# Optimization experiments

Measured on AMD Instinct MI355X. Metric: run time of the kernel, lower is better.

Reference implementation:

```python
import jax, jax.numpy as jnp
import numpy as np

B, S, L, C, H, D, CP = 32, 4, 64, 32, 4, 8, 16  # batch, tracks, bins, c_msa, heads, d_head, c_pair


def _ln(x, g, b, eps=1e-5):
    m = jnp.mean(x, axis=-1, keepdims=True)
    v = jnp.mean((x - m) ** 2, axis=-1, keepdims=True)
    return (x - m) / jnp.sqrt(v + eps) * g + b


def setup_inputs() -> dict:
    key = jax.random.key(0)
    ks = jax.random.split(key, 20)
    n = lambda k, shape, s=0.1: jax.random.normal(k, shape, jnp.float32) * s
    return dict(
        chip_ctcf=n(ks[0], (B, L), 1.0),
        chip_hac=n(ks[1], (B, L), 1.0),
        chip_me1=n(ks[2], (B, L), 1.0),
        chip_me3=n(ks[3], (B, L), 1.0),
        bulk_map=n(ks[4], (B, 1, L, L), 1.0),
        we_w=n(ks[5], (C, 1)), we_b=jnp.zeros((C,), jnp.float32),
        pos=n(ks[6], (1, 1, L, C)),
        mn_g=jnp.ones((C,), jnp.float32), mn_b=jnp.zeros((C,), jnp.float32),
        wq=n(ks[7], (C, C)), bq=jnp.zeros((C,), jnp.float32),
        wk=n(ks[8], (C, C)), bk=jnp.zeros((C,), jnp.float32),
        wv=n(ks[9], (C, C)), bv=jnp.zeros((C,), jnp.float32),
        wo=n(ks[10], (C, C)), bo=jnp.zeros((C,), jnp.float32),
        an_g=jnp.ones((C,), jnp.float32), an_b=jnp.zeros((C,), jnp.float32),
        conv_w=n(ks[11], (H,)), conv_b=jnp.zeros((H,), jnp.float32),
        gate_w=n(ks[12], (H, D, D)), gate_b=jnp.zeros((H, D), jnp.float32),
        pp_w=n(ks[13], (CP, C * C), 0.03), pp_b=jnp.zeros((CP,), jnp.float32),
        ada_g=jnp.ones((CP,), jnp.float32), ada_b=jnp.zeros((CP,), jnp.float32),
        ada_alpha=jnp.ones((1,), jnp.float32),
    )


def reference(chip_ctcf, chip_hac, chip_me1, chip_me3, bulk_map,
              we_w, we_b, pos, mn_g, mn_b,
              wq, bq, wk, bk, wv, bv, wo, bo, an_g, an_b,
              conv_w, conv_b, gate_w, gate_b,
              pp_w, pp_b, ada_g, ada_b, ada_alpha):
    # 1) build MSA: (B, S=4, L, C)
    signals = jnp.stack([chip_ctcf, chip_hac, chip_me1, chip_me3], axis=1)  # (B,S,L)
    msa = signals[..., None] * we_w[:, 0] + we_b                            # Linear(1,C)
    x = _ln(msa + pos, mn_g, mn_b)                                          # (B,S,L,C)

    # 2) row self-attention with bulk-derived per-head bias
    q = (x @ wq.T + bq).reshape(B, S, L, H, D)
    k = (x @ wk.T + bk).reshape(B, S, L, H, D)
    v = (x @ wv.T + bv).reshape(B, S, L, H, D)
    scores = jnp.einsum('bslhd,bsmhd->bshlm', q, k) / jnp.sqrt(jnp.float32(D))
    bias = bulk_map * conv_w.reshape(1, H, 1, 1) + conv_b.reshape(1, H, 1, 1)  # 1x1 conv -> (B,H,L,L)
    attn = jax.nn.softmax(scores + bias[:, None], axis=-1)                     # (B,S,H,L,L)
    out = jnp.einsum('bshlm,bsmhd->bshld', attn, v)
    gate = jax.nn.sigmoid(jnp.einsum('hcd,bshld->bshlc', gate_w, out)
                          + gate_b[None, None, :, None, :])
    out = out * gate
    out = out.transpose(0, 1, 3, 2, 4).reshape(B, S, L, C)
    out = out @ wo.T + bo
    x = _ln(x + out, an_g, an_b)                                            # post-attn LayerNorm

    # 3) outer-product (of max over tracks) pair features
    m = jnp.max(x, axis=1)                                                  # (B,L,C)
    pair = jnp.einsum('bic,bjd->bijcd', m, m).reshape(B, L, L, C * C)       # (B,L,L,1024)
    nrm = jnp.sqrt(jnp.sum(pair * pair, axis=-1, keepdims=True))
    pair = pair / jnp.maximum(nrm, 1e-6)                                    # F.normalize
    feat = pair @ pp_w.T + pp_b                                             # (B,L,L,CP)
    feat = feat + ada_alpha * _ln(feat, ada_g, ada_b)                       # AdaNorm
    feat = jax.nn.silu(feat)
    return feat.transpose(0, 3, 1, 2)                                       # (B,CP,L,L)
```

## Files before the change

### kernel.cpp

```cpp
#include <hip/hip_runtime.h>
#include <hip/hip_bf16.h>

#define NB 32
#define NS 4
#define NL 64
#define NC 32
#define NH 4
#define ND 8
#define NCP 16

using fp = const float* __restrict__;

__global__ __launch_bounds__(512) void k1_attn(
    fp ctcf, fp hac, fp me1, fp me3, fp bulk,
    fp we_w, fp we_b, fp pos, fp mn_g, fp mn_b,
    fp wq, fp bq, fp wk, fp bk, fp wv, fp bv,
    fp wo, fp bo, fp an_g, fp an_b,
    fp conv_w, fp conv_b, fp gate_w, fp gate_b,
    float* __restrict__ xpostT)
{
    __shared__ __align__(16) float q2[NL*36];
    __shared__ __align__(16) float k2[NL*36];
    __shared__ __align__(16) float v2[NL*36];
    __shared__ __align__(16) float x2[NL*36];
    __shared__ __align__(16) float a2[16*36];
    __shared__ float bs[16*65];
    __shared__ __align__(16) float ws_wq[NC*NC];
    __shared__ __align__(16) float ws_wk[NC*NC];
    __shared__ __align__(16) float ws_wv[NC*NC];
    __shared__ __align__(16) float ws_wo[NC*NC];
    __shared__ __align__(16) float ws_gw[NH*ND*ND];
    __shared__ __align__(16) float ws_par[352];

    const int t    = threadIdx.x;
    const int w    = t >> 6;
    const int l    = t & 63;
    const int bx   = blockIdx.x;
    const int b    = bx >> 4;
    const int s    = (bx >> 2) & 3;
    const int qtr  = bx & 3;

    if (t < 256) ((float4*)ws_wq)[t]       = ((const float4*)wq)[t];
    else         ((float4*)ws_wk)[t - 256] = ((const float4*)wk)[t - 256];

    if (t < 256) ((float4*)ws_wv)[t] = ((const float4*)wv)[t];
    else {
        int u = t - 256;
        if (u < 64) ((float4*)ws_gw)[u] = ((const float4*)gate_w)[u];
        else if (u < 152){
            int p = u - 64;
            const float* sp = (p < 8)  ? we_w : (p < 16) ? we_b
                            : (p < 24) ? mn_g : (p < 32) ? mn_b
                            : (p < 40) ? bq   : (p < 48) ? bk
                            : (p < 56) ? bv   : (p < 64) ? bo
                            : (p < 72) ? an_g : (p < 80) ? an_b : gate_b;
            ((float4*)ws_par)[p] = ((const float4*)sp)[p & 7];
        }
    }
    if (t < 256){
        int c = t >> 3, k4 = t & 7;
        ((float4*)ws_wo)[c*8 + (k4 ^ ((c >> 1) & 7))] = ((const float4*)wo)[t];
    }
    if (t < 256){
        float4 v = ((const float4*)(bulk + b*NL*NL + qtr*16*NL))[t];
        int row = t >> 4, col = (t & 15) << 2;
        float* dst = &bs[row*65 + col];
        dst[0] = v.x; dst[1] = v.y; dst[2] = v.z; dst[3] = v.w;
    }

    fp sigp = (s == 0) ? ctcf : (s == 1) ? hac : (s == 2) ? me1 : me3;
    const float sig = sigp[b*NL + l];
    __syncthreads();

    const float4* pws = (const float4*)ws_par;

    float x[NC];
    float mean = 0.f;
#pragma unroll
    for (int k4 = 0; k4 < 8; k4++){
        float4 ww = pws[k4];
        float4 wb = pws[8 + k4];
        float4 pp = ((const float4*)pos)[l*8 + k4];
        x[4*k4+0] = sig*ww.x + wb.x + pp.x;
        x[4*k4+1] = sig*ww.y + wb.y + pp.y;
        x[4*k4+2] = sig*ww.z + wb.z + pp.z;
        x[4*k4+3] = sig*ww.w + wb.w + pp.w;
        mean += x[4*k4+0] + x[4*k4+1] + x[4*k4+2] + x[4*k4+3];
    }
    mean *= (1.f/NC);
    float var = 0.f;
#pragma unroll
    for (int c = 0; c < NC; c++){ float d = x[c] - mean; var += d*d; }
    var *= (1.f/NC);
    float inv = rsqrtf(var + 1e-5f);
#pragma unroll
    for (int k4 = 0; k4 < 8; k4++){
        float4 gg = pws[16 + k4];
        float4 bb = pws[24 + k4];
        x[4*k4+0] = (x[4*k4+0] - mean)*inv*gg.x + bb.x;
        x[4*k4+1] = (x[4*k4+1] - mean)*inv*gg.y + bb.y;
        x[4*k4+2] = (x[4*k4+2] - mean)*inv*gg.z + bb.z;
        x[4*k4+3] = (x[4*k4+3] - mean)*inv*gg.w + bb.w;
    }

    {
        float aqv[4], akv[4], avv[4];
#pragma unroll
        for (int e4 = 0; e4 < 4; e4++){
            const int e = (w << 2) + e4;
            float aq = ws_par[128 + e], ak = ws_par[160 + e], av = ws_par[192 + e];
#pragma unroll
            for (int k4 = 0; k4 < 8; k4++){
                float4 wq4 = *(const float4*)&ws_wq[e*NC + 4*k4];
                float4 wk4 = *(const float4*)&ws_wk[e*NC + 4*k4];
                float4 wv4 = *(const float4*)&ws_wv[e*NC + 4*k4];
                float x0 = x[4*k4+0], x1 = x[4*k4+1], x2v = x[4*k4+2], x3 = x[4*k4+3];
                aq += wq4.x*x0 + wq4.y*x1 + wq4.z*x2v + wq4.w*x3;
                ak += wk4.x*x0 + wk4.y*x1 + wk4.z*x2v + wk4.w*x3;
                av += wv4.x*x0 + wv4.y*x1 + wv4.z*x2v + wv4.w*x3;
            }
            aqv[e4] = aq; akv[e4] = ak; avv[e4] = av;
        }
        const int slt = ((w >> 1) ^ (l >> 4));
        const int kh  = (w & 1);
        const int off = l*36 + slt*8 + kh*4;
        *(float4*)&q2[off] = make_float4(aqv[0], aqv[1], aqv[2], aqv[3]);
        *(float4*)&k2[off] = make_float4(akv[0], akv[1], akv[2], akv[3]);
        *(float4*)&v2[off] = make_float4(avv[0], avv[1], avv[2], avv[3]);
        float xa = 0.f, xb2 = 0.f, xc = 0.f, xd = 0.f;
#pragma unroll
        for (int ww = 0; ww < 8; ww++)
            if (ww == w){ xa = x[4*ww]; xb2 = x[4*ww+1]; xc = x[4*ww+2]; xd = x[4*ww+3]; }
        *(float4*)&x2[l*36 + ((w ^ (l >> 4)) << 2)] = make_float4(xa, xb2, xc, xd);
    }
    __syncthreads();

    {
        const int h   = w >> 1;
        const int sub = ((w & 1) << 6) | l;
        const int rl  = sub >> 3;
        const int q8  = sub & 7;
        const int r   = qtr*16 + rl;
        const int m0  = q8 << 3;

        const int qoff = r*36 + ((h ^ (r >> 4)) << 3);
        float4 qa = *(const float4*)&q2[qoff];
        float4 qb = *(const float4*)&q2[qoff + 4];

        const float rs8 = 0.35355339059327373f;
        const float cw = conv_w[h], cb = conv_b[h];
        const float* bsr = &bs[rl*65];
        float srow[8];
        float mx = -1e30f;
#pragma unroll
        for (int mi = 0; mi < 8; mi++){
            int m  = m0 + mi;
            int kb = m*36 + ((h ^ (m >> 4)) << 3);
            float4 ka  = *(const float4*)&k2[kb];
            float4 kb4 = *(const float4*)&k2[kb + 4];
            float dot = qa.x*ka.x + qa.y*ka.y + qa.z*ka.z + qa.w*ka.w
                      + qb.x*kb4.x + qb.y*kb4.y + qb.z*kb4.z + qb.w*kb4.w;
            float vv = dot*rs8 + bsr[m]*cw + cb;
            srow[mi] = vv;
            mx = fmaxf(mx, vv);
        }
        mx = fmaxf(mx, __shfl_xor(mx, 1));
        mx = fmaxf(mx, __shfl_xor(mx, 2));
        mx = fmaxf(mx, __shfl_xor(mx, 4));
        float sm = 0.f;
#pragma unroll
        for (int mi = 0; mi < 8; mi++){ srow[mi] = __expf(srow[mi] - mx); sm += srow[mi]; }
        sm += __shfl_xor(sm, 1);
        sm += __shfl_xor(sm, 2);
        sm += __shfl_xor(sm, 4);
        float is = 1.f / sm;

        float4 oa = make_float4(0.f,0.f,0.f,0.f);
        float4 ob = make_float4(0.f,0.f,0.f,0.f);
#pragma unroll
        for (int mi = 0; mi < 8; mi++){
            int m  = m0 + mi;
            int vb = m*36 + ((h ^ (m >> 4)) << 3);
            float a = srow[mi] * is;
            float4 va  = *(const float4*)&v2[vb];
            float4 vb4 = *(const float4*)&v2[vb + 4];
            oa.x += a*va.x;  oa.y += a*va.y;  oa.z += a*va.z;  oa.w += a*va.w;
            ob.x += a*vb4.x; ob.y += a*vb4.y; ob.z += a*vb4.z; ob.w += a*vb4.w;
        }
#define RED3(f) f += __shfl_xor(f, 1); f += __shfl_xor(f, 2); f += __shfl_xor(f, 4);
        RED3(oa.x) RED3(oa.y) RED3(oa.z) RED3(oa.w)
        RED3(ob.x) RED3(ob.y) RED3(ob.z) RED3(ob.w)
#undef RED3

        const float* gwl = &ws_gw[(h*ND + q8)*ND];
        float4 g1 = *(const float4*)gwl;
        float4 g2 = *(const float4*)(gwl + 4);
        float g = ws_par[320 + h*ND + q8]
                + g1.x*oa.x + g1.y*oa.y + g1.z*oa.z + g1.w*oa.w
                + g2.x*ob.x + g2.y*ob.y + g2.z*ob.z + g2.w*ob.w;
        float oc = oa.x;
        if (q8 == 1) oc = oa.y;
        if (q8 == 2) oc = oa.z;
        if (q8 == 3) oc = oa.w;
        if (q8 == 4) oc = ob.x;
        if (q8 == 5) oc = ob.y;
        if (q8 == 6) oc = ob.z;
        if (q8 == 7) oc = ob.w;
        a2[rl*36 + h*8 + q8] = oc * (1.f/(1.f + __expf(-g)));
    }
    __syncthreads();

    {
        const int r3 = t >> 5;
        const int c  = t & 31;
        const int rg = qtr*16 + r3;
        float acc = ws_par[224 + c];
#pragma unroll
        for (int k4 = 0; k4 < 8; k4++){
            float4 av = *(const float4*)&a2[r3*36 + (k4 << 2)];
            float4 w1 = ((const float4*)ws_wo)[c*8 + (k4 ^ ((c >> 1) & 7))];
            acc += av.x*w1.x + av.y*w1.y + av.z*w1.z + av.w*w1.w;
        }
        float xr = x2[rg*36 + (((c >> 2) ^ (rg >> 4)) << 2) + (c & 3)];
        float val = xr + acc;
        float ps = val, pq = val*val;
        ps += __shfl_xor(ps, 1);  pq += __shfl_xor(pq, 1);
        ps += __shfl_xor(ps, 2);  pq += __shfl_xor(pq, 2);
        ps += __shfl_xor(ps, 4);  pq += __shfl_xor(pq, 4);
        ps += __shfl_xor(ps, 8);  pq += __shfl_xor(pq, 8);
        ps += __shfl_xor(ps, 16); pq += __shfl_xor(pq, 16);
        float mn = ps * (1.f/NC);
        float vr = pq * (1.f/NC) - mn*mn;
        float iv = rsqrtf(vr + 1e-5f);
        xpostT[((b*NS + s)*NL + rg)*NC + c] =
            (val - mn)*iv*ws_par[256 + c] + ws_par[288 + c];
    }
}

__global__ __launch_bounds__(256) void k23_pair(
    const float* __restrict__ xpostT, fp pp_w,
    fp pp_b, fp ada_g, fp ada_b, fp ada_alpha,
    float* __restrict__ out)
{
    __shared__ float ppws[8*NC*NC];
    __shared__ float mh[NC*66];
    __shared__ float u[NCP*4*NC];
    __shared__ float nrm_s[NL];

    const int b  = blockIdx.x >> 4;
    const int it = blockIdx.x & 15;
    const int t  = threadIdx.x;
    const int w  = t >> 6;
    const int j  = t & 63;

    float4 s1[8];
#pragma unroll
    for (int k = 0; k < 8; k++) s1[k] = ((const float4*)pp_w)[k*256 + t];

    const float4* xb4 = (const float4*)(xpostT + b*NS*NL*NC);
#pragma unroll
    for (int k = 0; k < 2; k++){
        int idx = k*256 + t;
        float4 v0 = xb4[idx];
        float4 v1 = xb4[512  + idx];
        float4 v2 = xb4[1024 + idx];
        float4 v3 = xb4[1536 + idx];
        float m0 = fmaxf(fmaxf(v0.x, v1.x), fmaxf(v2.x, v3.x));
        float m1 = fmaxf(fmaxf(v0.y, v1.y), fmaxf(v2.y, v3.y));
        float m2 = fmaxf(fmaxf(v0.z, v1.z), fmaxf(v2.z, v3.z));
        float m3 = fmaxf(fmaxf(v0.w, v1.w), fmaxf(v2.w, v3.w));
        int l = idx >> 3, c4 = idx & 7;
        mh[(4*c4+0)*66 + l] = m0;
        mh[(4*c4+1)*66 + l] = m1;
        mh[(4*c4+2)*66 + l] = m2;
        mh[(4*c4+3)*66 + l] = m3;
    }
#pragma unroll
    for (int k = 0; k < 8; k++) ((float4*)ppws)[k*256 + t] = s1[k];
    __syncthreads();

    if (t < NL){
        float sq = 0.f;
#pragma unroll
        for (int c = 0; c < NC; c++){ float v = mh[c*66 + t]; sq += v*v; }
        nrm_s[t] = sqrtf(sq);
    }

    float4 s2[8];
#pragma unroll
    for (int k = 0; k < 8; k++) s2[k] = ((const float4*)pp_w)[2048 + k*256 + t];

#pragma unroll
    for (int loop = 0; loop < 4; loop++){
        int idx = loop*256 + t;
        int d  = idx & 31;
        int ip = (idx >> 5) & 3;
        int pl = idx >> 7;
        int i  = it*4 + ip;
        float acc = 0.f;
#pragma unroll
        for (int c = 0; c < NC; c++)
            acc += mh[c*66 + i] * ppws[pl*1024 + c*32 + d];
        u[pl*128 + ip*32 + d] = acc;
    }
    __syncthreads();
#pragma unroll
    for (int k = 0; k < 8; k++) ((float4*)ppws)[k*256 + t] = s2[k];
    __syncthreads();

#pragma unroll
    for (int loop = 0; loop < 4; loop++){
        int idx = loop*256 + t;
        int d  = idx & 31;
        int ip = (idx >> 5) & 3;
        int pl = idx >> 7;
        int i  = it*4 + ip;
        float acc = 0.f;
#pragma unroll
        for (int c = 0; c < NC; c++)
            acc += mh[c*66 + i] * ppws[pl*1024 + c*32 + d];
        u[(8 + pl)*128 + ip*32 + d] = acc;
    }
    __syncthreads();

    float md[NC];
#pragma unroll
    for (int c = 0; c < NC; c++) md[c] = mh[c*66 + j];

    const int i = it*4 + w;
    float f[NCP];
#pragma unroll
    for (int p = 0; p < NCP; p++){
        float a = 0.f;
#pragma unroll
        for (int k4 = 0; k4 < 8; k4++){
            float4 uv = *(const float4*)&u[p*128 + w*32 + (k4 << 2)];
            a += uv.x*md[4*k4+0] + uv.y*md[4*k4+1] + uv.z*md[4*k4+2] + uv.w*md[4*k4+3];
        }
        f[p] = a;
    }

    const float sc = 1.f / fmaxf(nrm_s[i] * nrm_s[j], 1e-6f);
    const float alpha = ada_alpha[0];
    float fsum = 0.f, fsq = 0.f;
#pragma unroll
    for (int p = 0; p < NCP; p++){
        float v = f[p]*sc + pp_b[p];
        f[p] = v; fsum += v; fsq += v*v;
    }
    float fmean = fsum * (1.f/NCP);
    float fvar  = fsq * (1.f/NCP) - fmean*fmean;
    float finv  = rsqrtf(fvar + 1e-5f);
#pragma unroll
    for (int p = 0; p < NCP; p++){
        float v = f[p] + alpha * ((f[p] - fmean)*finv*ada_g[p] + ada_b[p]);
        out[((b*NCP + p)*NL + i)*NL + j] = v / (1.f + __expf(-v));
    }
}

extern "C" void kernel_launch(void* const* d_in, const int* in_sizes, int n_in,
                              void* d_out, int out_size, void* d_ws, size_t ws_size,
                              hipStream_t stream)
{
    float* xpostT = (float*)d_ws;

    k1_attn<<<NB*NS*4, 512, 0, stream>>>(
        (fp)d_in[0], (fp)d_in[1], (fp)d_in[2], (fp)d_in[3], (fp)d_in[4],
        (fp)d_in[5], (fp)d_in[6], (fp)d_in[7], (fp)d_in[8], (fp)d_in[9],
        (fp)d_in[10], (fp)d_in[11], (fp)d_in[12], (fp)d_in[13], (fp)d_in[14], (fp)d_in[15],
        (fp)d_in[16], (fp)d_in[17], (fp)d_in[18], (fp)d_in[19],
        (fp)d_in[20], (fp)d_in[21], (fp)d_in[22], (fp)d_in[23], xpostT);

    k23_pair<<<NB*16, 256, 0, stream>>>(
        xpostT, (fp)d_in[24], (fp)d_in[25], (fp)d_in[26], (fp)d_in[27], (fp)d_in[28],
        (float*)d_out);
}
```

Measured before the change: 144.8 us.

## Split attention into half-row blocks of 1024 threads and vectorize pair projection

```diff
diff --git a/kernel.cpp b/kernel.cpp
--- a/kernel.cpp
+++ b/kernel.cpp
@@ -11,7 +11,7 @@
 
 using fp = const float* __restrict__;
 
-__global__ __launch_bounds__(512) void k1_attn(
+__global__ __launch_bounds__(1024) void k1_attn(
     fp ctcf, fp hac, fp me1, fp me3, fp bulk,
     fp we_w, fp we_b, fp pos, fp mn_g, fp mn_b,
     fp wq, fp bq, fp wk, fp bk, fp wv, fp bv,
@@ -23,8 +23,8 @@
     __shared__ __align__(16) float k2[NL*36];
     __shared__ __align__(16) float v2[NL*36];
     __shared__ __align__(16) float x2[NL*36];
-    __shared__ __align__(16) float a2[16*36];
-    __shared__ float bs[16*65];
+    __shared__ __align__(16) float a2[NL*36];
+    __shared__ float bs[32*65];
     __shared__ __align__(16) float ws_wq[NC*NC];
     __shared__ __align__(16) float ws_wk[NC*NC];
     __shared__ __align__(16) float ws_wv[NC*NC];
@@ -33,37 +33,35 @@
     __shared__ __align__(16) float ws_par[352];
 
     const int t    = threadIdx.x;
-    const int w    = t >> 6;
+    const int w2   = t >> 6;
     const int l    = t & 63;
     const int bx   = blockIdx.x;
-    const int b    = bx >> 4;
-    const int s    = (bx >> 2) & 3;
-    const int qtr  = bx & 3;
-
-    if (t < 256) ((float4*)ws_wq)[t]       = ((const float4*)wq)[t];
-    else         ((float4*)ws_wk)[t - 256] = ((const float4*)wk)[t - 256];
-
-    if (t < 256) ((float4*)ws_wv)[t] = ((const float4*)wv)[t];
+    const int b    = bx >> 3;
+    const int s    = (bx >> 1) & 3;
+    const int half = bx & 1;
+
+    if      (t < 256) ((float4*)ws_wq)[t]       = ((const float4*)wq)[t];
+    else if (t < 512) ((float4*)ws_wk)[t - 256] = ((const float4*)wk)[t - 256];
+    else if (t < 768) ((float4*)ws_wv)[t - 512] = ((const float4*)wv)[t - 512];
     else {
-        int u = t - 256;
-        if (u < 64) ((float4*)ws_gw)[u] = ((const float4*)gate_w)[u];
-        else if (u < 152){
-            int p = u - 64;
-            const float* sp = (p < 8)  ? we_w : (p < 16) ? we_b
-                            : (p < 24) ? mn_g : (p < 32) ? mn_b
-                            : (p < 40) ? bq   : (p < 48) ? bk
-                            : (p < 56) ? bv   : (p < 64) ? bo
-                            : (p < 72) ? an_g : (p < 80) ? an_b : gate_b;
-            ((float4*)ws_par)[p] = ((const float4*)sp)[p & 7];
-        }
-    }
-    if (t < 256){
-        int c = t >> 3, k4 = t & 7;
-        ((float4*)ws_wo)[c*8 + (k4 ^ ((c >> 1) & 7))] = ((const float4*)wo)[t];
-    }
-    if (t < 256){
-        float4 v = ((const float4*)(bulk + b*NL*NL + qtr*16*NL))[t];
-        int row = t >> 4, col = (t & 15) << 2;
+        int u = t - 768;
+        int c = u >> 3, k4 = u & 7;
+        ((float4*)ws_wo)[c*8 + (k4 ^ ((c >> 1) & 7))] = ((const float4*)wo)[u];
+    }
+    if (t < 64) ((float4*)ws_gw)[t] = ((const float4*)gate_w)[t];
+    else if (t < 152){
+        int p = t - 64;
+        const float* sp = (p < 8)  ? we_w : (p < 16) ? we_b
+                        : (p < 24) ? mn_g : (p < 32) ? mn_b
+                        : (p < 40) ? bq   : (p < 48) ? bk
+                        : (p < 56) ? bv   : (p < 64) ? bo
+                        : (p < 72) ? an_g : (p < 80) ? an_b : gate_b;
+        ((float4*)ws_par)[p] = ((const float4*)sp)[p & 7];
+    }
+    if (t >= 512){
+        int idx = t - 512;
+        float4 v = ((const float4*)(bulk + b*NL*NL + half*32*NL))[idx];
+        int row = idx >> 4, col = (idx & 15) << 2;
         float* dst = &bs[row*65 + col];
         dst[0] = v.x; dst[1] = v.y; dst[2] = v.z; dst[3] = v.w;
     }
@@ -104,10 +102,10 @@
     }
 
     {
-        float aqv[4], akv[4], avv[4];
-#pragma unroll
-        for (int e4 = 0; e4 < 4; e4++){
-            const int e = (w << 2) + e4;
+        float aqv[2], akv[2], avv[2];
+#pragma unroll
+        for (int e2 = 0; e2 < 2; e2++){
+            const int e = (w2 << 1) + e2;
             float aq = ws_par[128 + e], ak = ws_par[160 + e], av = ws_par[192 + e];
 #pragma unroll
             for (int k4 = 0; k4 < 8; k4++){
@@ -119,28 +117,30 @@
                 ak += wk4.x*x0 + wk4.y*x1 + wk4.z*x2v + wk4.w*x3;
                 av += wv4.x*x0 + wv4.y*x1 + wv4.z*x2v + wv4.w*x3;
             }
-            aqv[e4] = aq; akv[e4] = ak; avv[e4] = av;
-        }
-        const int slt = ((w >> 1) ^ (l >> 4));
-        const int kh  = (w & 1);
-        const int off = l*36 + slt*8 + kh*4;
-        *(float4*)&q2[off] = make_float4(aqv[0], aqv[1], aqv[2], aqv[3]);
-        *(float4*)&k2[off] = make_float4(akv[0], akv[1], akv[2], akv[3]);
-        *(float4*)&v2[off] = make_float4(avv[0], avv[1], avv[2], avv[3]);
-        float xa = 0.f, xb2 = 0.f, xc = 0.f, xd = 0.f;
-#pragma unroll
-        for (int ww = 0; ww < 8; ww++)
-            if (ww == w){ xa = x[4*ww]; xb2 = x[4*ww+1]; xc = x[4*ww+2]; xd = x[4*ww+3]; }
-        *(float4*)&x2[l*36 + ((w ^ (l >> 4)) << 2)] = make_float4(xa, xb2, xc, xd);
-    }
-    __syncthreads();
-
-    {
-        const int h   = w >> 1;
-        const int sub = ((w & 1) << 6) | l;
+            aqv[e2] = aq; akv[e2] = ak; avv[e2] = av;
+        }
+        const int h    = w2 >> 2;
+        const int slth = h ^ (l >> 4);
+        const int off  = l*36 + (slth << 3) + ((w2 & 3) << 1);
+        *(float2*)&q2[off] = make_float2(aqv[0], aqv[1]);
+        *(float2*)&k2[off] = make_float2(akv[0], akv[1]);
+        *(float2*)&v2[off] = make_float2(avv[0], avv[1]);
+        if (w2 < 8){
+            float xa = 0.f, xb2 = 0.f, xc = 0.f, xd = 0.f;
+#pragma unroll
+            for (int ww = 0; ww < 8; ww++)
+                if (ww == w2){ xa = x[4*ww]; xb2 = x[4*ww+1]; xc = x[4*ww+2]; xd = x[4*ww+3]; }
+            *(float4*)&x2[l*36 + ((w2 ^ (l >> 4)) << 2)] = make_float4(xa, xb2, xc, xd);
+        }
+    }
+    __syncthreads();
+
+    {
+        const int h   = w2 >> 2;
+        const int sub = ((w2 & 3) << 6) | l;
         const int rl  = sub >> 3;
         const int q8  = sub & 7;
-        const int r   = qtr*16 + rl;
+        const int r   = half*32 + rl;
         const int m0  = q8 << 3;
 
         const int qoff = r*36 + ((h ^ (r >> 4)) << 3);
@@ -206,18 +206,18 @@
         if (q8 == 5) oc = ob.y;
         if (q8 == 6) oc = ob.z;
         if (q8 == 7) oc = ob.w;
-        a2[rl*36 + h*8 + q8] = oc * (1.f/(1.f + __expf(-g)));
+        a2[r*36 + h*8 + q8] = oc * (1.f/(1.f + __expf(-g)));
     }
     __syncthreads();
 
     {
         const int r3 = t >> 5;
         const int c  = t & 31;
-        const int rg = qtr*16 + r3;
+        const int rg = half*32 + r3;
         float acc = ws_par[224 + c];
 #pragma unroll
         for (int k4 = 0; k4 < 8; k4++){
-            float4 av = *(const float4*)&a2[r3*36 + (k4 << 2)];
+            float4 av = *(const float4*)&a2[rg*36 + (k4 << 2)];
             float4 w1 = ((const float4*)ws_wo)[c*8 + (k4 ^ ((c >> 1) & 7))];
             acc += av.x*w1.x + av.y*w1.y + av.z*w1.z + av.w*w1.w;
         }
@@ -290,36 +290,40 @@
 #pragma unroll
     for (int k = 0; k < 8; k++) s2[k] = ((const float4*)pp_w)[2048 + k*256 + t];
 
-#pragma unroll
-    for (int loop = 0; loop < 4; loop++){
-        int idx = loop*256 + t;
-        int d  = idx & 31;
-        int ip = (idx >> 5) & 3;
-        int pl = idx >> 7;
-        int i  = it*4 + ip;
-        float acc = 0.f;
-#pragma unroll
-        for (int c = 0; c < NC; c++)
-            acc += mh[c*66 + i] * ppws[pl*1024 + c*32 + d];
-        u[pl*128 + ip*32 + d] = acc;
+    const int dq  = t & 7;
+    const int ipz = (t >> 3) & 3;
+    const int plz = t >> 5;
+    const int iz  = it*4 + ipz;
+    {
+        float4 acc = make_float4(0.f, 0.f, 0.f, 0.f);
+        const float*  mrow = &mh[iz];
+        const float4* wrow = (const float4*)&ppws[plz*1024 + (dq << 2)];
+#pragma unroll
+        for (int c = 0; c < NC; c++){
+            float  mhv = mrow[c*66];
+            float4 wv  = wrow[c*8];
+            acc.x += mhv*wv.x; acc.y += mhv*wv.y;
+            acc.z += mhv*wv.z; acc.w += mhv*wv.w;
+        }
+        *(float4*)&u[plz*128 + ipz*32 + (dq << 2)] = acc;
     }
     __syncthreads();
 #pragma unroll
     for (int k = 0; k < 8; k++) ((float4*)ppws)[k*256 + t] = s2[k];
     __syncthreads();
 
-#pragma unroll
-    for (int loop = 0; loop < 4; loop++){
-        int idx = loop*256 + t;
-        int d  = idx & 31;
-        int ip = (idx >> 5) & 3;
-        int pl = idx >> 7;
-        int i  = it*4 + ip;
-        float acc = 0.f;
-#pragma unroll
-        for (int c = 0; c < NC; c++)
-            acc += mh[c*66 + i] * ppws[pl*1024 + c*32 + d];
-        u[(8 + pl)*128 + ip*32 + d] = acc;
+    {
+        float4 acc = make_float4(0.f, 0.f, 0.f, 0.f);
+        const float*  mrow = &mh[iz];
+        const float4* wrow = (const float4*)&ppws[plz*1024 + (dq << 2)];
+#pragma unroll
+        for (int c = 0; c < NC; c++){
+            float  mhv = mrow[c*66];
+            float4 wv  = wrow[c*8];
+            acc.x += mhv*wv.x; acc.y += mhv*wv.y;
+            acc.z += mhv*wv.z; acc.w += mhv*wv.w;
+        }
+        *(float4*)&u[(8 + plz)*128 + ipz*32 + (dq << 2)] = acc;
     }
     __syncthreads();
 
@@ -364,7 +368,7 @@
 {
     float* xpostT = (float*)d_ws;
 
-    k1_attn<<<NB*NS*4, 512, 0, stream>>>(
+    k1_attn<<<NB*NS*2, 1024, 0, stream>>>(
         (fp)d_in[0], (fp)d_in[1], (fp)d_in[2], (fp)d_in[3], (fp)d_in[4],
         (fp)d_in[5], (fp)d_in[6], (fp)d_in[7], (fp)d_in[8], (fp)d_in[9],
         (fp)d_in[10], (fp)d_in[11], (fp)d_in[12], (fp)d_in[13], (fp)d_in[14], (fp)d_in[15],
```

Result: faster. 137.7 us (-4.9%).
